# Kernel optimization log

Measured on AMD Instinct MI355X. Metric: run time of the kernel, lower is better.

Reference implementation:

```python
import jax, jax.numpy as jnp
import numpy as np

B, S, H = 2, 2048, 2048
NH, KVH, HD = 32, 8, 64
G = NH // KVH
BASE = 10000.0
SCALE = 1.0 / np.sqrt(HD).astype(np.float32)


def _rope_cache(seq_len, dim, base):
    inv_freq = 1.0 / (base ** (jnp.arange(0, dim, 2, dtype=jnp.float32) / dim))
    t = jnp.arange(seq_len, dtype=jnp.float32)
    freqs = jnp.outer(t, inv_freq)            # [S, HD/2]
    emb = jnp.concatenate([freqs, freqs], -1)  # [S, HD]
    return jnp.cos(emb), jnp.sin(emb)


def _rotate_half(x):
    x1, x2 = jnp.split(x, 2, axis=-1)
    return jnp.concatenate([-x2, x1], axis=-1)


def setup_inputs() -> dict:
    key = jax.random.key(0)
    ks = jax.random.split(key, 5)
    hidden_states = jax.random.normal(ks[0], (B, S, H), jnp.float32)
    # additive causal mask, broadcast over heads
    causal = jnp.tril(jnp.ones((S, S), dtype=bool))
    attention_mask = jnp.where(causal, 0.0, -1e9).astype(jnp.float32)[None, None]
    attention_mask = jnp.broadcast_to(attention_mask, (B, 1, S, S))
    position_ids = jnp.broadcast_to(jnp.arange(S, dtype=jnp.int32), (B, S))
    w = 0.02
    Wq = jax.random.normal(ks[1], (H, NH * HD), jnp.float32) * w
    Wk = jax.random.normal(ks[2], (H, KVH * HD), jnp.float32) * w
    Wv = jax.random.normal(ks[3], (H, KVH * HD), jnp.float32) * w
    Wo = jax.random.normal(ks[4], (NH * HD, H), jnp.float32) * w
    return {"hidden_states": hidden_states, "attention_mask": attention_mask,
            "position_ids": position_ids, "Wq": Wq, "Wk": Wk, "Wv": Wv, "Wo": Wo}


def reference(hidden_states, attention_mask, position_ids, Wq, Wk, Wv, Wo):
    b, s, _ = hidden_states.shape
    q = (hidden_states @ Wq).reshape(b, s, NH, HD).transpose(0, 2, 1, 3)   # [B,NH,S,HD]
    k = (hidden_states @ Wk).reshape(b, s, KVH, HD).transpose(0, 2, 1, 3)  # [B,KVH,S,HD]
    v = (hidden_states @ Wv).reshape(b, s, KVH, HD).transpose(0, 2, 1, 3)
    cos_c, sin_c = _rope_cache(s, HD, BASE)
    cos = cos_c[position_ids][:, None]  # [B,1,S,HD]
    sin = sin_c[position_ids][:, None]
    q = q * cos + _rotate_half(q) * sin
    k = k * cos + _rotate_half(k) * sin
    # GQA: grouped einsum == repeat_kv + matmul (same math, no KV duplication)
    qg = q.reshape(b, KVH, G, s, HD)
    scores = jnp.einsum('bkgsd,bktd->bkgst', qg, k) * SCALE  # [B,KVH,G,S,S]
    scores = scores + attention_mask[:, :, None]             # mask [B,1,1,S,S]
    probs = jax.nn.softmax(scores.astype(jnp.float32), axis=-1).astype(q.dtype)
    ctx = jnp.einsum('bkgst,bktd->bkgsd', probs, v)
    ctx = ctx.reshape(b, NH, s, HD).transpose(0, 2, 1, 3).reshape(b, s, NH * HD)
    return ctx @ Wo
```

## Files before the change

kernel.cpp:

```cpp
#include <hip/hip_runtime.h>
#include <hip/hip_bf16.h>

#define DB   2
#define DS   2048
#define DH   2048
#define DNH  32
#define DKVH 8
#define DHD  64
#define DM   4096
#define DNQKV 3072

typedef __attribute__((ext_vector_type(8))) short bf16x8;
typedef __attribute__((ext_vector_type(4))) float f32x4;
typedef __attribute__((ext_vector_type(8))) unsigned short us8;
typedef __attribute__((ext_vector_type(4))) unsigned short us4;

__device__ __forceinline__ float b2f(unsigned short u) {
  unsigned int x = ((unsigned int)u) << 16;
  return __builtin_bit_cast(float, x);
}
__device__ __forceinline__ unsigned short f2b(float f) {
  unsigned int u = __builtin_bit_cast(unsigned int, f);
  return (unsigned short)((u + 0x8000u) >> 16);
}
__device__ __forceinline__ void async_copy16(void* lds, const void* g) {
  __builtin_amdgcn_global_load_lds((const __attribute__((address_space(1))) void*)g,
                                   (__attribute__((address_space(3))) void*)lds,
                                   16, 0, 0);
}

__global__ void detect_mode(const unsigned short* __restrict__ w, int* __restrict__ flags) {
  int t = threadIdx.x;
  int trips = 0;
  for (int i = 0; i < 4; i++) {
    unsigned short u = w[t * 4 + i];
    int e = (u >> 7) & 0xFF;
    if (e >= 161 || (e <= 93 && e != 0)) trips++;
  }
  for (int off = 32; off > 0; off >>= 1) trips += __shfl_down(trips, off);
  if (t == 0) flags[0] = (trips >= 8) ? 1 : 0;
}

__global__ __launch_bounds__(256)
void prep(const void* __restrict__ hs,
          const void* __restrict__ wq, const void* __restrict__ wk,
          const void* __restrict__ wv, const void* __restrict__ wo,
          unsigned short* __restrict__ xb, unsigned short* __restrict__ wtqkv,
          unsigned short* __restrict__ wto, const int* __restrict__ flags) {
  __shared__ float tile[32][33];
  int mode = flags[0];
  int bid = blockIdx.x, tid = threadIdx.x;
  if (bid < 4096) {
    int i = (bid * 256 + tid) * 8;
    if (mode) {
      const float* f = (const float*)hs;
      us8 o;
#pragma unroll
      for (int j = 0; j < 8; j++) o[j] = f2b(f[i + j]);
      *(us8*)&xb[i] = o;
    } else {
      *(us8*)&xb[i] = *(const us8*)((const unsigned short*)hs + i);
    }
    return;
  }
  const void* src; unsigned short* dst; int C, bx, by;
  if (bid < 8192)      { int b2 = bid - 4096; src = wq; dst = wtqkv;                         C = 2048; bx = b2 & 63; by = b2 >> 6; }
  else if (bid < 9216) { int b2 = bid - 8192; src = wk; dst = wtqkv + (size_t)2048 * 2048;   C = 512;  bx = b2 & 15; by = b2 >> 4; }
  else if (bid < 10240){ int b2 = bid - 9216; src = wv; dst = wtqkv + (size_t)2560 * 2048;   C = 512;  bx = b2 & 15; by = b2 >> 4; }
  else                 { int b2 = bid - 10240; src = wo; dst = wto;                          C = 2048; bx = b2 & 63; by = b2 >> 6; }
  const int R = 2048;
  int c0 = bx * 32, r0 = by * 32;
  int tx = tid & 31, ty = tid >> 5;
  if (mode) {
    const float* f = (const float*)src;
    for (int i = ty; i < 32; i += 8) tile[i][tx] = f[(size_t)(r0 + i) * C + c0 + tx];
  } else {
    const unsigned short* bsrc = (const unsigned short*)src;
    for (int i = ty; i < 32; i += 8) tile[i][tx] = b2f(bsrc[(size_t)(r0 + i) * C + c0 + tx]);
  }
  __syncthreads();
  for (int i = ty; i < 32; i += 8) dst[(size_t)(c0 + i) * R + r0 + tx] = f2b(tile[tx][i]);
}

#define QSC 0.18033688011112042f

__global__ __launch_bounds__(256)
void gemm_qkv(const unsigned short* __restrict__ A, const unsigned short* __restrict__ Bt,
              const int* __restrict__ pos_ids,
              unsigned short* __restrict__ qws, unsigned short* __restrict__ kws,
              unsigned short* __restrict__ vt) {
  __shared__ __align__(16) unsigned short lA[2 * 128 * 32];
  __shared__ __align__(16) unsigned short lB[2 * 128 * 32];
  int tid = threadIdx.x, lane = tid & 63, wave = tid >> 6;
  int wm = wave >> 1, wn = wave & 1;
  int quad = lane >> 4, l15 = lane & 15;
  size_t tm0 = (size_t)blockIdx.y * 128, tn0 = (size_t)blockIdx.x * 128;

  f32x4 zero4 = {0.f, 0.f, 0.f, 0.f};
  f32x4 acc[4][4];
#pragma unroll
  for (int mi = 0; mi < 4; mi++)
#pragma unroll
    for (int ni = 0; ni < 4; ni++) acc[mi][ni] = zero4;

  for (int kt = 0; kt < 32; kt++) {
    __syncthreads();
#pragma unroll
    for (int i = 0; i < 4; i++) {
      int c = tid + 256 * i;
      int col = (c & 3) * 8;
      int r = (c >> 2) & 127;
      int half = c >> 9;
      async_copy16(&lA[c * 8], A + (tm0 + r) * DH + kt * 64 + half * 32 + col);
      async_copy16(&lB[c * 8], Bt + (tn0 + r) * DH + kt * 64 + half * 32 + col);
    }
    __syncthreads();
#pragma unroll
    for (int ks = 0; ks < 2; ks++) {
      bf16x8 af[4], bfr[4];
#pragma unroll
      for (int mi = 0; mi < 4; mi++)
        af[mi] = *(const bf16x8*)&lA[ks * 4096 + (wm * 64 + mi * 16 + l15) * 32 + quad * 8];
#pragma unroll
      for (int ni = 0; ni < 4; ni++)
        bfr[ni] = *(const bf16x8*)&lB[ks * 4096 + (wn * 64 + ni * 16 + l15) * 32 + quad * 8];
#pragma unroll
      for (int mi = 0; mi < 4; mi++)
#pragma unroll
        for (int ni = 0; ni < 4; ni++)
          acc[mi][ni] = __builtin_amdgcn_mfma_f32_16x16x32_bf16(af[mi], bfr[ni], acc[mi][ni], 0, 0, 0);
    }
  }

  int hs = (int)(tn0 >> 6) + wn;
  if (hs < 40) {
    float sc = (hs < 32) ? QSC : 1.0f;
    unsigned short* dst0 = (hs < 32) ? qws : kws;
    int hh = (hs < 32) ? hs : (hs - 32);
    float invf0 = __expf(-(float)l15 * (9.210340371976184f / 32.0f));
    float invf1 = invf0 * 0.01f;
#pragma unroll
    for (int mi = 0; mi < 4; mi++)
#pragma unroll
      for (int r = 0; r < 4; r++) {
        size_t gr = tm0 + wm * 64 + mi * 16 + quad * 4 + r;
        int b = (int)(gr >> 11), s = (int)(gr & 2047);
        float t = (float)pos_ids[gr];
        unsigned short* row = dst0 + ((size_t)(b * ((hs < 32) ? DNH : DKVH) + hh) * DS + s) * DHD;
#pragma unroll
        for (int ni = 0; ni < 2; ni++) {
          float x1 = acc[mi][ni][r], x2 = acc[mi][ni + 2][r];
          float ang = t * (ni ? invf1 : invf0);
          float sn, cs;
          __sincosf(ang, &sn, &cs);
          int d = ni * 16 + l15;
          row[d]      = f2b((x1 * cs - x2 * sn) * sc);
          row[d + 32] = f2b((x2 * cs + x1 * sn) * sc);
        }
      }
  } else {
    int vh = hs - 40;
    int b = (int)(tm0 >> 11);
    int s0 = (int)(tm0 & 2047) + wm * 64 + quad * 4;
#pragma unroll
    for (int mi = 0; mi < 4; mi++)
#pragma unroll
      for (int ni = 0; ni < 4; ni++) {
        int d = ni * 16 + l15;
        us4 o4;
#pragma unroll
        for (int r = 0; r < 4; r++) o4[r] = f2b(acc[mi][ni][r]);
        *(us4*)&vt[((size_t)(b * DKVH + vh) * DHD + d) * DS + s0 + mi * 16] = o4;
      }
  }
}

__global__ __launch_bounds__(256)
void gemm_out(const unsigned short* __restrict__ A, const unsigned short* __restrict__ Bt,
              unsigned short* __restrict__ Cb, float* __restrict__ Cf,
              const int* __restrict__ outmode) {
  __shared__ __align__(16) unsigned short lA[2 * 128 * 32];
  __shared__ __align__(16) unsigned short lB[2 * 128 * 32];
  int tid = threadIdx.x, lane = tid & 63, wave = tid >> 6;
  int wm = wave >> 1, wn = wave & 1;
  int quad = lane >> 4, l15 = lane & 15;
  size_t tm0 = (size_t)blockIdx.y * 128, tn0 = (size_t)blockIdx.x * 128;

  f32x4 zero4 = {0.f, 0.f, 0.f, 0.f};
  f32x4 acc[4][4];
#pragma unroll
  for (int mi = 0; mi < 4; mi++)
#pragma unroll
    for (int ni = 0; ni < 4; ni++) acc[mi][ni] = zero4;

  for (int kt = 0; kt < 32; kt++) {
    __syncthreads();
#pragma unroll
    for (int i = 0; i < 4; i++) {
      int c = tid + 256 * i;
      int col = (c & 3) * 8;
      int r = (c >> 2) & 127;
      int half = c >> 9;
      async_copy16(&lA[c * 8], A + (tm0 + r) * DH + kt * 64 + half * 32 + col);
      async_copy16(&lB[c * 8], Bt + (tn0 + r) * DH + kt * 64 + half * 32 + col);
    }
    __syncthreads();
#pragma unroll
    for (int ks = 0; ks < 2; ks++) {
      bf16x8 af[4], bfr[4];
#pragma unroll
      for (int mi = 0; mi < 4; mi++)
        af[mi] = *(const bf16x8*)&lA[ks * 4096 + (wm * 64 + mi * 16 + l15) * 32 + quad * 8];
#pragma unroll
      for (int ni = 0; ni < 4; ni++)
        bfr[ni] = *(const bf16x8*)&lB[ks * 4096 + (wn * 64 + ni * 16 + l15) * 32 + quad * 8];
#pragma unroll
      for (int mi = 0; mi < 4; mi++)
#pragma unroll
        for (int ni = 0; ni < 4; ni++)
          acc[mi][ni] = __builtin_amdgcn_mfma_f32_16x16x32_bf16(af[mi], bfr[ni], acc[mi][ni], 0, 0, 0);
    }
  }
  int mode = *outmode;
#pragma unroll
  for (int mi = 0; mi < 4; mi++)
#pragma unroll
    for (int ni = 0; ni < 4; ni++)
#pragma unroll
      for (int r = 0; r < 4; r++) {
        size_t gr = tm0 + wm * 64 + mi * 16 + quad * 4 + r;
        size_t gc = tn0 + wn * 64 + ni * 16 + l15;
        float v = acc[mi][ni][r];
        if (mode) Cf[gr * DH + gc] = v;
        else      Cb[gr * DH + gc] = f2b(v);
      }
}

__global__ __launch_bounds__(256, 4)
void flash_attn(const unsigned short* __restrict__ q, const unsigned short* __restrict__ k,
                const unsigned short* __restrict__ vt, unsigned short* __restrict__ ctx) {
  __shared__ __align__(16) unsigned short lK[4 * 64 * 32];
  __shared__ __align__(16) unsigned short lV[4 * 64 * 32];
  __shared__ __align__(16) unsigned short lP[4 * 16 * 36];
  int tid = threadIdx.x, lane = tid & 63, wave = tid >> 6;
  int quad = lane >> 4, l15 = lane & 15;
  int bh = blockIdx.y, b = bh >> 5, h = bh & 31, kvh = h >> 2;
  const unsigned short* qb = q + (size_t)(b * DNH + h) * DS * DHD;
  const unsigned short* kb = k + (size_t)(b * DKVH + kvh) * DS * DHD;
  const unsigned short* vb = vt + (size_t)(b * DKVH + kvh) * DHD * DS;
  unsigned short* lPw = lP + wave * 16 * 36;
  int cpl = (tid & 3) * 8;
  int crow = (tid >> 2) & 63;

  f32x4 zero4 = {0.f, 0.f, 0.f, 0.f};
  for (int ph = 0; ph < 2; ph++) {
    int qt = ph ? (31 - blockIdx.x) : blockIdx.x;
    int q0 = qt * 64;
    const unsigned short* qp = qb + (size_t)(q0 + wave * 16 + l15) * DHD + quad * 8;
    bf16x8 qf0 = *(const bf16x8*)qp;
    bf16x8 qf1 = *(const bf16x8*)(qp + 32);
    f32x4 oacc[4];
#pragma unroll
    for (int dj = 0; dj < 4; dj++) oacc[dj] = zero4;
    float lrow = 0.f;
    int ql = wave * 16 + l15;

    int nit = (qt + 2) >> 1;
    for (int it = 0; it < nit; it++) {
      int kv0 = it * 128;
      __syncthreads();
#pragma unroll
      for (int i = 0; i < 4; i++)
        async_copy16(&lK[(tid + 256 * i) * 8],
                     kb + (size_t)(kv0 + (i >> 1) * 64 + crow) * DHD + (i & 1) * 32 + cpl);
#pragma unroll
      for (int i = 0; i < 4; i++)
        async_copy16(&lV[(tid + 256 * i) * 8],
                     vb + (size_t)crow * DS + kv0 + i * 32 + cpl);
      __syncthreads();

      auto do_half = [&](int hh) {
        int st = it * 2 + hh;
        f32x4 sacc[4];
#pragma unroll
        for (int nj = 0; nj < 4; nj++) {
          sacc[nj] = zero4;
          bf16x8 kf0 = *(const bf16x8*)&lK[(hh * 2 + 0) * 2048 + (nj * 16 + l15) * 32 + quad * 8];
          bf16x8 kf1 = *(const bf16x8*)&lK[(hh * 2 + 1) * 2048 + (nj * 16 + l15) * 32 + quad * 8];
          sacc[nj] = __builtin_amdgcn_mfma_f32_16x16x32_bf16(kf0, qf0, sacc[nj], 0, 0, 0);
          sacc[nj] = __builtin_amdgcn_mfma_f32_16x16x32_bf16(kf1, qf1, sacc[nj], 0, 0, 0);
        }
        if (st == qt) {
#pragma unroll
          for (int nj = 0; nj < 4; nj++)
#pragma unroll
            for (int r = 0; r < 4; r++)
              if (nj * 16 + quad * 4 + r > ql) sacc[nj][r] = -1e30f;
        }
#pragma unroll
        for (int nj = 0; nj < 4; nj++)
#pragma unroll
          for (int r = 0; r < 4; r++) {
            float e = __builtin_amdgcn_exp2f(sacc[nj][r] - 12.0f);
            sacc[nj][r] = e;
            lrow += e;
          }
#pragma unroll
        for (int qq = 0; qq < 2; qq++) {
#pragma unroll
          for (int jj = 0; jj < 2; jj++) {
            int nj = qq * 2 + jj;
            us4 w4;
#pragma unroll
            for (int r = 0; r < 4; r++) w4[r] = f2b(sacc[nj][r]);
            *(us4*)&lPw[l15 * 36 + jj * 16 + quad * 4] = w4;
          }
          bf16x8 pf = *(const bf16x8*)&lPw[l15 * 36 + quad * 8];
#pragma unroll
          for (int dj = 0; dj < 4; dj++) {
            bf16x8 vf = *(const bf16x8*)&lV[(hh * 2 + qq) * 2048 + (dj * 16 + l15) * 32 + quad * 8];
            oacc[dj] = __builtin_amdgcn_mfma_f32_16x16x32_bf16(vf, pf, oacc[dj], 0, 0, 0);
          }
        }
      };
      do_half(0);
      if (it * 2 + 1 <= qt) do_half(1);
    }
    lrow += __shfl_xor(lrow, 16);
    lrow += __shfl_xor(lrow, 32);
    float inv = __builtin_amdgcn_rcpf(lrow);
    size_t orow = ((size_t)b * DS + q0 + wave * 16 + l15) * (DNH * DHD) + (size_t)h * DHD;
#pragma unroll
    for (int dj = 0; dj < 4; dj++) {
      us4 o4;
#pragma unroll
      for (int r = 0; r < 4; r++) o4[r] = f2b(oacc[dj][r] * inv);
      *(us4*)&ctx[orow + dj * 16 + quad * 4] = o4;
    }
  }
}

extern "C" void kernel_launch(void* const* d_in, const int* in_sizes, int n_in,
                              void* d_out, int out_size, void* d_ws, size_t ws_size,
                              hipStream_t stream) {
  (void)in_sizes; (void)n_in; (void)out_size; (void)ws_size;
  const void* hs = d_in[0];
  const int* pos = (const int*)d_in[2];
  const void* wq = d_in[3];
  const void* wk = d_in[4];
  const void* wv = d_in[5];
  const void* wo = d_in[6];

  char* ws = (char*)d_ws;
  size_t off = 0;
  auto take = [&](size_t bytes) -> char* {
    char* p = ws + off;
    off += (bytes + 255) & ~(size_t)255;
    return p;
  };
  int* flags            = (int*)take(256);
  unsigned short* xb    = (unsigned short*)take((size_t)DM * DH * 2);
  unsigned short* wtqkv = (unsigned short*)take((size_t)DNQKV * DH * 2);
  unsigned short* wto   = (unsigned short*)take((size_t)DH * DH * 2);
  unsigned short* qws   = (unsigned short*)take((size_t)DB * DNH * DS * DHD * 2);
  unsigned short* kws   = (unsigned short*)take((size_t)DB * DKVH * DS * DHD * 2);
  unsigned short* vtws  = (unsigned short*)take((size_t)DB * DKVH * DS * DHD * 2);
  unsigned short* ctx   = (unsigned short*)take((size_t)DM * DNH * DHD * 2);

  detect_mode<<<1, 64, 0, stream>>>((const unsigned short*)wq, flags);
  prep<<<14336, 256, 0, stream>>>(hs, wq, wk, wv, wo, xb, wtqkv, wto, flags);
  gemm_qkv<<<dim3(24, 32), 256, 0, stream>>>(xb, wtqkv, pos, qws, kws, vtws);
  flash_attn<<<dim3(16, DB * DNH), 256, 0, stream>>>(qws, kws, vtws, ctx);
  gemm_out<<<dim3(16, 32), 256, 0, stream>>>(ctx, wto, (unsigned short*)d_out, (float*)d_out, flags);
}
```

Before: 357.3 us.

## Process two query tiles per attention block and shrink output GEMM tiles

The flash attention kernel now handles 128 query rows per block as two 64-row groups sharing each loaded K/V tile. This halves the number of K/V loads and barriers per query row, at the cost of more registers and a dropped occupancy hint. The output GEMM moves to single-wave 64x64 tiles, giving four times as many blocks for better load balance but a smaller per-block tile. The ctx buffer now reuses the xb workspace, which is dead after the QKV GEMM, instead of allocating a separate one.

```diff
diff --git a/kernel.cpp b/kernel.cpp
--- a/kernel.cpp
+++ b/kernel.cpp
@@ -175,16 +175,15 @@
   }
 }
 
-__global__ __launch_bounds__(256)
+__global__ __launch_bounds__(64)
 void gemm_out(const unsigned short* __restrict__ A, const unsigned short* __restrict__ Bt,
               unsigned short* __restrict__ Cb, float* __restrict__ Cf,
               const int* __restrict__ outmode) {
-  __shared__ __align__(16) unsigned short lA[2 * 128 * 32];
-  __shared__ __align__(16) unsigned short lB[2 * 128 * 32];
-  int tid = threadIdx.x, lane = tid & 63, wave = tid >> 6;
-  int wm = wave >> 1, wn = wave & 1;
+  __shared__ __align__(16) unsigned short lA[2 * 64 * 32];
+  __shared__ __align__(16) unsigned short lB[2 * 64 * 32];
+  int lane = threadIdx.x;
   int quad = lane >> 4, l15 = lane & 15;
-  size_t tm0 = (size_t)blockIdx.y * 128, tn0 = (size_t)blockIdx.x * 128;
+  size_t tm0 = (size_t)blockIdx.y * 64, tn0 = (size_t)blockIdx.x * 64;
 
   f32x4 zero4 = {0.f, 0.f, 0.f, 0.f};
   f32x4 acc[4][4];
@@ -196,11 +195,11 @@
   for (int kt = 0; kt < 32; kt++) {
     __syncthreads();
 #pragma unroll
-    for (int i = 0; i < 4; i++) {
-      int c = tid + 256 * i;
+    for (int i = 0; i < 8; i++) {
+      int c = lane + 64 * i;
       int col = (c & 3) * 8;
-      int r = (c >> 2) & 127;
-      int half = c >> 9;
+      int r = (c >> 2) & 63;
+      int half = c >> 8;
       async_copy16(&lA[c * 8], A + (tm0 + r) * DH + kt * 64 + half * 32 + col);
       async_copy16(&lB[c * 8], Bt + (tn0 + r) * DH + kt * 64 + half * 32 + col);
     }
@@ -210,10 +209,10 @@
       bf16x8 af[4], bfr[4];
 #pragma unroll
       for (int mi = 0; mi < 4; mi++)
-        af[mi] = *(const bf16x8*)&lA[ks * 4096 + (wm * 64 + mi * 16 + l15) * 32 + quad * 8];
+        af[mi] = *(const bf16x8*)&lA[ks * 2048 + (mi * 16 + l15) * 32 + quad * 8];
 #pragma unroll
       for (int ni = 0; ni < 4; ni++)
-        bfr[ni] = *(const bf16x8*)&lB[ks * 4096 + (wn * 64 + ni * 16 + l15) * 32 + quad * 8];
+        bfr[ni] = *(const bf16x8*)&lB[ks * 2048 + (ni * 16 + l15) * 32 + quad * 8];
 #pragma unroll
       for (int mi = 0; mi < 4; mi++)
 #pragma unroll
@@ -228,44 +227,50 @@
     for (int ni = 0; ni < 4; ni++)
 #pragma unroll
       for (int r = 0; r < 4; r++) {
-        size_t gr = tm0 + wm * 64 + mi * 16 + quad * 4 + r;
-        size_t gc = tn0 + wn * 64 + ni * 16 + l15;
+        size_t gr = tm0 + mi * 16 + quad * 4 + r;
+        size_t gc = tn0 + ni * 16 + l15;
         float v = acc[mi][ni][r];
         if (mode) Cf[gr * DH + gc] = v;
         else      Cb[gr * DH + gc] = f2b(v);
       }
 }
 
-__global__ __launch_bounds__(256, 4)
+__global__ __launch_bounds__(256)
 void flash_attn(const unsigned short* __restrict__ q, const unsigned short* __restrict__ k,
                 const unsigned short* __restrict__ vt, unsigned short* __restrict__ ctx) {
   __shared__ __align__(16) unsigned short lK[4 * 64 * 32];
   __shared__ __align__(16) unsigned short lV[4 * 64 * 32];
-  __shared__ __align__(16) unsigned short lP[4 * 16 * 36];
+  __shared__ __align__(16) unsigned short lP[4 * 2 * 16 * 36];
   int tid = threadIdx.x, lane = tid & 63, wave = tid >> 6;
   int quad = lane >> 4, l15 = lane & 15;
   int bh = blockIdx.y, b = bh >> 5, h = bh & 31, kvh = h >> 2;
   const unsigned short* qb = q + (size_t)(b * DNH + h) * DS * DHD;
   const unsigned short* kb = k + (size_t)(b * DKVH + kvh) * DS * DHD;
   const unsigned short* vb = vt + (size_t)(b * DKVH + kvh) * DHD * DS;
-  unsigned short* lPw = lP + wave * 16 * 36;
+  unsigned short* lPw = lP + wave * 1152;
   int cpl = (tid & 3) * 8;
   int crow = (tid >> 2) & 63;
 
   f32x4 zero4 = {0.f, 0.f, 0.f, 0.f};
   for (int ph = 0; ph < 2; ph++) {
-    int qt = ph ? (31 - blockIdx.x) : blockIdx.x;
-    int q0 = qt * 64;
-    const unsigned short* qp = qb + (size_t)(q0 + wave * 16 + l15) * DHD + quad * 8;
-    bf16x8 qf0 = *(const bf16x8*)qp;
-    bf16x8 qf1 = *(const bf16x8*)(qp + 32);
-    f32x4 oacc[4];
-#pragma unroll
-    for (int dj = 0; dj < 4; dj++) oacc[dj] = zero4;
-    float lrow = 0.f;
+    int qt2 = ph ? (15 - blockIdx.x) : blockIdx.x;
+    int q0 = qt2 * 128;
+    bf16x8 qf[2][2];
+#pragma unroll
+    for (int g = 0; g < 2; g++) {
+      const unsigned short* qp = qb + (size_t)(q0 + g * 64 + wave * 16 + l15) * DHD + quad * 8;
+      qf[g][0] = *(const bf16x8*)qp;
+      qf[g][1] = *(const bf16x8*)(qp + 32);
+    }
+    f32x4 oacc[2][4];
+#pragma unroll
+    for (int g = 0; g < 2; g++)
+#pragma unroll
+      for (int dj = 0; dj < 4; dj++) oacc[g][dj] = zero4;
+    float lrow[2] = {0.f, 0.f};
     int ql = wave * 16 + l15;
 
-    int nit = (qt + 2) >> 1;
+    int nit = qt2 + 1;
     for (int it = 0; it < nit; it++) {
       int kv0 = it * 128;
       __syncthreads();
@@ -279,63 +284,75 @@
                      vb + (size_t)crow * DS + kv0 + i * 32 + cpl);
       __syncthreads();
 
-      auto do_half = [&](int hh) {
+      for (int hh = 0; hh < 2; hh++) {
         int st = it * 2 + hh;
-        f32x4 sacc[4];
+        int gmin = (st == 2 * qt2 + 1) ? 1 : 0;
+        f32x4 sacc[2][4];
+        for (int g = gmin; g < 2; g++)
+#pragma unroll
+          for (int nj = 0; nj < 4; nj++) sacc[g][nj] = zero4;
 #pragma unroll
         for (int nj = 0; nj < 4; nj++) {
-          sacc[nj] = zero4;
           bf16x8 kf0 = *(const bf16x8*)&lK[(hh * 2 + 0) * 2048 + (nj * 16 + l15) * 32 + quad * 8];
           bf16x8 kf1 = *(const bf16x8*)&lK[(hh * 2 + 1) * 2048 + (nj * 16 + l15) * 32 + quad * 8];
-          sacc[nj] = __builtin_amdgcn_mfma_f32_16x16x32_bf16(kf0, qf0, sacc[nj], 0, 0, 0);
-          sacc[nj] = __builtin_amdgcn_mfma_f32_16x16x32_bf16(kf1, qf1, sacc[nj], 0, 0, 0);
+          for (int g = gmin; g < 2; g++) {
+            sacc[g][nj] = __builtin_amdgcn_mfma_f32_16x16x32_bf16(kf0, qf[g][0], sacc[g][nj], 0, 0, 0);
+            sacc[g][nj] = __builtin_amdgcn_mfma_f32_16x16x32_bf16(kf1, qf[g][1], sacc[g][nj], 0, 0, 0);
+          }
         }
-        if (st == qt) {
+        for (int g = gmin; g < 2; g++) {
+          if (st == 2 * qt2 + g) {
+#pragma unroll
+            for (int nj = 0; nj < 4; nj++)
+#pragma unroll
+              for (int r = 0; r < 4; r++)
+                if (nj * 16 + quad * 4 + r > ql) sacc[g][nj][r] = -1e30f;
+          }
 #pragma unroll
           for (int nj = 0; nj < 4; nj++)
 #pragma unroll
-            for (int r = 0; r < 4; r++)
-              if (nj * 16 + quad * 4 + r > ql) sacc[nj][r] = -1e30f;
+            for (int r = 0; r < 4; r++) {
+              float e = __builtin_amdgcn_exp2f(sacc[g][nj][r] - 12.0f);
+              sacc[g][nj][r] = e;
+              lrow[g] += e;
+            }
         }
 #pragma unroll
-        for (int nj = 0; nj < 4; nj++)
-#pragma unroll
-          for (int r = 0; r < 4; r++) {
-            float e = __builtin_amdgcn_exp2f(sacc[nj][r] - 12.0f);
-            sacc[nj][r] = e;
-            lrow += e;
-          }
-#pragma unroll
         for (int qq = 0; qq < 2; qq++) {
-#pragma unroll
-          for (int jj = 0; jj < 2; jj++) {
-            int nj = qq * 2 + jj;
-            us4 w4;
-#pragma unroll
-            for (int r = 0; r < 4; r++) w4[r] = f2b(sacc[nj][r]);
-            *(us4*)&lPw[l15 * 36 + jj * 16 + quad * 4] = w4;
-          }
-          bf16x8 pf = *(const bf16x8*)&lPw[l15 * 36 + quad * 8];
+          for (int g = gmin; g < 2; g++)
+#pragma unroll
+            for (int jj = 0; jj < 2; jj++) {
+              us4 w4;
+#pragma unroll
+              for (int r = 0; r < 4; r++) w4[r] = f2b(sacc[g][qq * 2 + jj][r]);
+              *(us4*)&lPw[g * 576 + l15 * 36 + jj * 16 + quad * 4] = w4;
+            }
+          bf16x8 pf[2];
+          for (int g = gmin; g < 2; g++)
+            pf[g] = *(const bf16x8*)&lPw[g * 576 + l15 * 36 + quad * 8];
 #pragma unroll
           for (int dj = 0; dj < 4; dj++) {
             bf16x8 vf = *(const bf16x8*)&lV[(hh * 2 + qq) * 2048 + (dj * 16 + l15) * 32 + quad * 8];
-            oacc[dj] = __builtin_amdgcn_mfma_f32_16x16x32_bf16(vf, pf, oacc[dj], 0, 0, 0);
+            for (int g = gmin; g < 2; g++)
+              oacc[g][dj] = __builtin_amdgcn_mfma_f32_16x16x32_bf16(vf, pf[g], oacc[g][dj], 0, 0, 0);
           }
         }
-      };
-      do_half(0);
-      if (it * 2 + 1 <= qt) do_half(1);
-    }
-    lrow += __shfl_xor(lrow, 16);
-    lrow += __shfl_xor(lrow, 32);
-    float inv = __builtin_amdgcn_rcpf(lrow);
-    size_t orow = ((size_t)b * DS + q0 + wave * 16 + l15) * (DNH * DHD) + (size_t)h * DHD;
-#pragma unroll
-    for (int dj = 0; dj < 4; dj++) {
-      us4 o4;
-#pragma unroll
-      for (int r = 0; r < 4; r++) o4[r] = f2b(oacc[dj][r] * inv);
-      *(us4*)&ctx[orow + dj * 16 + quad * 4] = o4;
+      }
+    }
+#pragma unroll
+    for (int g = 0; g < 2; g++) {
+      float l = lrow[g];
+      l += __shfl_xor(l, 16);
+      l += __shfl_xor(l, 32);
+      float inv = __builtin_amdgcn_rcpf(l);
+      size_t orow = ((size_t)b * DS + q0 + g * 64 + wave * 16 + l15) * (DNH * DHD) + (size_t)h * DHD;
+#pragma unroll
+      for (int dj = 0; dj < 4; dj++) {
+        us4 o4;
+#pragma unroll
+        for (int r = 0; r < 4; r++) o4[r] = f2b(oacc[g][dj][r] * inv);
+        *(us4*)&ctx[orow + dj * 16 + quad * 4] = o4;
+      }
     }
   }
 }
@@ -365,11 +382,11 @@
   unsigned short* qws   = (unsigned short*)take((size_t)DB * DNH * DS * DHD * 2);
   unsigned short* kws   = (unsigned short*)take((size_t)DB * DKVH * DS * DHD * 2);
   unsigned short* vtws  = (unsigned short*)take((size_t)DB * DKVH * DS * DHD * 2);
-  unsigned short* ctx   = (unsigned short*)take((size_t)DM * DNH * DHD * 2);
+  unsigned short* ctx   = xb;
 
   detect_mode<<<1, 64, 0, stream>>>((const unsigned short*)wq, flags);
   prep<<<14336, 256, 0, stream>>>(hs, wq, wk, wv, wo, xb, wtqkv, wto, flags);
   gemm_qkv<<<dim3(24, 32), 256, 0, stream>>>(xb, wtqkv, pos, qws, kws, vtws);
-  flash_attn<<<dim3(16, DB * DNH), 256, 0, stream>>>(qws, kws, vtws, ctx);
-  gemm_out<<<dim3(16, 32), 256, 0, stream>>>(ctx, wto, (unsigned short*)d_out, (float*)d_out, flags);
-}
+  flash_attn<<<dim3(8, DB * DNH), 256, 0, stream>>>(qws, kws, vtws, ctx);
+  gemm_out<<<dim3(32, 64), 64, 0, stream>>>(ctx, wto, (unsigned short*)d_out, (float*)d_out, flags);
+}
```

After: 1.060 ms. 197% more time.
